# Optimization experiments

Measured on AMD Instinct MI355X. Metric: run time of the kernel, lower is better.

Reference implementation:

```python
import jax, jax.numpy as jnp
import numpy as np

NH, NB, E, R, K, SU = 64, 384, 1024, 1024, 16, 64  # humans, boxes, enc size, repr size, cardinality, sub-repr
C, P, SPA = 256, 7, 36
NUM_ITER = 2


def _ln(x, g, b):
    m = jnp.mean(x, -1, keepdims=True)
    v = jnp.mean((x - m) ** 2, -1, keepdims=True)
    return (x - m) / jnp.sqrt(v + 1e-5) * g + b


def setup_inputs():
    key = jax.random.key(0)
    it = iter(jax.random.split(key, 48))
    def w(shape, scale=0.02):
        return jax.random.normal(next(it), shape, dtype=jnp.float32) * scale
    z = lambda *s: jnp.zeros(s, jnp.float32)
    return {
        "box_feats": jax.random.normal(next(it), (NB, C, P, P), dtype=jnp.float32),
        "spatial_raw": jax.random.uniform(next(it), (NH * NB, SPA), dtype=jnp.float32),
        "features3": jax.random.normal(next(it), (1, C, P, P), dtype=jnp.float32),
        "Wb1": w((C * P * P, E)), "bb1": z(E), "Wb2": w((E, E)), "bb2": z(E),
        "Ws1": w((SPA, 128)), "bs1": z(128), "Ws2": w((128, 256)), "bs2": z(256),
        "Ws3": w((256, 1024)), "bs3": z(1024),
        "Wadj": w((R, 1)), "badj": z(1),
        "gh": jnp.ones((E,), jnp.float32), "bh": z(E),
        "go": jnp.ones((E,), jnp.float32), "bo": z(E),
        "A1": w((K, 2 * E, SU)), "Ab1": z(K, SU), "A2": w((K, 1024, SU)), "Ab2": z(K, SU),
        "A3": w((K, SU, R)), "Ab3": z(K, R),
        "G1": w((K, 256, SU)), "Gb1": z(K, SU), "G2": w((K, 1024, SU)), "Gb2": z(K, SU),
        "G3": w((K, SU, R)), "Gb3": z(K, R),
        "S1": w((K, E, SU)), "Sb1": z(K, SU), "S2": w((K, 1024, SU)), "Sb2": z(K, SU),
        "S3": w((K, SU, R)), "Sb3": z(K, R),
        "O1": w((K, E, SU)), "Ob1": z(K, SU), "O2": w((K, 1024, SU)), "Ob2": z(K, SU),
        "O3": w((K, SU, R)), "Ob3": z(K, R),
        "n_h": NH,
    }


def _forward(box_feats, spatial_raw, features3, Wb1, bb1, Wb2, bb2, Ws1, bs1, Ws2, bs2, Ws3, bs3,
             Wadj, badj, gh, bh, go, bo, A1, Ab1, A2, Ab2, A3, Ab3, G1, Gb1, G2, Gb2, G3, Gb3,
             S1, Sb1, S2, Sb2, S3, Sb3, O1, Ob1, O2, Ob2, O3, Ob3, n_h):
    n = box_feats.shape[0]
    # box_head: Flatten -> Linear -> ReLU -> Linear -> ReLU
    enc = jax.nn.relu(jax.nn.relu(box_feats.reshape(n, -1) @ Wb1 + bb1) @ Wb2 + bb2)  # [n, E]
    h, o = enc[:n_h], enc
    # spatial_head MLP on flat pairs (pair p = i*n + j, human i, object j)
    sp = spatial_raw
    for W, b in ((Ws1, bs1), (Ws2, bs2), (Ws3, bs3)):
        sp = jax.nn.relu(sp @ W + b)                      # [n_h*n, 1024]
    spr = sp.reshape(n_h, n, -1)
    gfeat = features3.mean((2, 3))                        # AdaptiveAvgPool2d(1) -> [1, 256]

    def mbf(app, W1, b1, W2, b2, W3, b3):
        # MultiBranchFusion over flat pairs, K branches vectorized as batched GEMMs
        a = jnp.einsum('pa,kau->kpu', app, W1) + b1[:, None, :]
        s = jnp.einsum('ps,ksu->kpu', sp, W2) + b2[:, None, :]
        m = jax.nn.relu(a * s)                            # [K, P, sub]
        return jax.nn.relu(jnp.einsum('kpu,kur->pr', m, W3) + b3.sum(0))

    def pair_app(hh, oo):
        return jnp.concatenate([jnp.repeat(hh, n, axis=0), jnp.tile(oo, (n_h, 1))], axis=1)

    adj = jnp.ones((n_h, n), sp.dtype)
    for _ in range(NUM_ITER):
        wts = mbf(pair_app(h, o), A1, Ab1, A2, Ab2, A3, Ab3)      # [P, R]
        adj = (wts @ Wadj + badj).reshape(n_h, n)
        # MessageMBF object->subject (_forward_object_nodes): output [n_h, n, R], no final relu
        ao = jnp.einsum('na,kau->knu', o, O1) + Ob1[:, None, :]
        so = jnp.einsum('hns,ksu->khnu', spr, O2) + Ob2[:, None, None, :]
        m_o2s = jnp.einsum('khnu,kur->hnr', jax.nn.relu(ao[:, None] * so), O3) + Ob3.sum(0)
        h = _ln(h + jax.nn.relu(jnp.sum(jax.nn.softmax(adj, 1)[..., None] * m_o2s, axis=1)), gh, bh)
        # MessageMBF subject->object (_forward_human_nodes): output [n, n_h, R]
        ah = jnp.einsum('ha,kau->khu', h, S1) + Sb1[:, None, :]
        sh = jnp.einsum('hns,ksu->khnu', spr, S2) + Sb2[:, None, None, :]
        m_s2o = jnp.einsum('khnu,kur->nhr', jax.nn.relu(ah[:, :, None, :] * sh), S3) + Sb3.sum(0)
        o = _ln(o + jax.nn.relu(jnp.sum(jax.nn.softmax(adj.T, 1)[..., None] * m_s2o, axis=1)), go, bo)

    attn = mbf(pair_app(h, o), A1, Ab1, A2, Ab2, A3, Ab3)          # [P, R]
    gp = jnp.broadcast_to(gfeat, (sp.shape[0], gfeat.shape[1]))
    attn_g = mbf(gp, G1, Gb1, G2, Gb2, G3, Gb3)                    # [P, R]
    return jnp.concatenate([attn, attn_g], axis=1)                 # [P, 2R]


def reference(box_feats, spatial_raw, features3, Wb1, bb1, Wb2, bb2, Ws1, bs1, Ws2, bs2, Ws3, bs3,
              Wadj, badj, gh, bh, go, bo, A1, Ab1, A2, Ab2, A3, Ab3, G1, Gb1, G2, Gb2, G3, Gb3,
              S1, Sb1, S2, Sb2, S3, Sb3, O1, Ob1, O2, Ob2, O3, Ob3, n_h):
    return _forward(box_feats, spatial_raw, features3, Wb1, bb1, Wb2, bb2, Ws1, bs1, Ws2, bs2, Ws3, bs3,
                    Wadj, badj, gh, bh, go, bo, A1, Ab1, A2, Ab2, A3, Ab3, G1, Gb1, G2, Gb2, G3, Gb3,
                    S1, Sb1, S2, Sb2, S3, Sb3, O1, Ob1, O2, Ob2, O3, Ob3, n_h)
```

## Files before the change

### kernel.cpp

```cpp
#include <hip/hip_runtime.h>
#include <hip/hip_bf16.h>
#include <cstdint>
#include <cstddef>

#define NH    64
#define NB    384
#define EDIM  1024
#define PAIRS (NH*NB)
#define SPA   36

using in_t  = float;
using out_t = float;
using sb_t  = __hip_bfloat16;

typedef short bf16x8 __attribute__((ext_vector_type(8)));
typedef float f32x4  __attribute__((ext_vector_type(4)));

static __device__ __forceinline__ float cvt(float x){ return x; }
static __device__ __forceinline__ float cvt(__hip_bfloat16 x){ return __bfloat162float(x); }
static __device__ __forceinline__ void stv(float* p, float v){ *p = v; }
static __device__ __forceinline__ void stv(__hip_bfloat16* p, float v){ *p = __float2bfloat16(v); }

static __device__ __forceinline__ float b2f(unsigned short u){
  union { unsigned int i; float f; } x; x.i = ((unsigned int)u)<<16; return x.f;
}

typedef const __attribute__((address_space(1))) void* as1_t;
typedef __attribute__((address_space(3))) void* as3_t;
static __device__ __forceinline__ void gl_lds16(const void* g, void* l){
  __builtin_amdgcn_global_load_lds((as1_t)g, (as3_t)l, 16, 0, 0);
}

#define POOL_BB1   0
#define POOL_BB2   1024
#define POOL_BS1   2048
#define POOL_BS2   2176
#define POOL_BS3   2432
#define POOL_AB1   3456
#define POOL_GB1   4480
#define POOL_SB1   5504
#define POOL_OB1   6528
#define POOL_B2ALL 7552
#define POOL_AB3S  11648
#define POOL_GB3S  12672
#define POOL_SB3S  13696
#define POOL_OB3S  14720
#define POOL_GFEAT 15744
#define POOL_TOTAL 16000

template<int EPI, int RELU, typename TC>
__global__ __launch_bounds__(256)
void gemm_mfma(int M, int N, int KS, int lda, int ldb,
               const sb_t* __restrict__ A,
               const sb_t* __restrict__ Bt,
               const float* __restrict__ bias,
               TC* __restrict__ C, int ldc, int coff, long long strideCz,
               const float* __restrict__ Wadj,
               const float* __restrict__ ab3s,
               float* __restrict__ adjOut)
{
  __shared__ alignas(16) short lA[2][128*32];
  __shared__ alignas(16) short lB[2][128*32];
  const int tid = threadIdx.x;
  const int w = tid >> 6, l = tid & 63;
  const int m0 = blockIdx.x * 128, n0 = blockIdx.y * 128;
  const int wr = w >> 1, wc = w & 1;
  const int Koff = blockIdx.z * KS;

  const int srow = w*32 + (l>>2);
  const int scol = (l&3)*8;
  const sb_t* gA = A  + (size_t)(m0 + srow)*(size_t)lda + Koff + scol;
  const sb_t* gB = Bt + (size_t)(n0 + srow)*(size_t)ldb + Koff + scol;
  short* lA0 = &lA[0][(w*32)*32];
  short* lA1 = &lA[1][(w*32)*32];
  short* lB0 = &lB[0][(w*32)*32];
  short* lB1 = &lB[1][(w*32)*32];

  f32x4 acc[4][4];
  const f32x4 zz = {0.f,0.f,0.f,0.f};
  #pragma unroll
  for (int i=0;i<4;++i)
    #pragma unroll
    for (int j=0;j<4;++j) acc[i][j] = zz;

  const int fr  = l & 15;
  const int fko = (l >> 4) * 8;

  for (int k0 = 0; k0 < KS; k0 += 64) {
    gl_lds16(gA + k0,               lA0);
    gl_lds16(gA + k0 + 16*lda,      lA0 + 16*32);
    gl_lds16(gA + k0 + 32,          lA1);
    gl_lds16(gA + k0 + 32 + 16*lda, lA1 + 16*32);
    gl_lds16(gB + k0,               lB0);
    gl_lds16(gB + k0 + 16*ldb,      lB0 + 16*32);
    gl_lds16(gB + k0 + 32,          lB1);
    gl_lds16(gB + k0 + 32 + 16*ldb, lB1 + 16*32);
    __syncthreads();
    #pragma unroll
    for (int kh=0; kh<2; ++kh) {
      bf16x8 af[4], bfv[4];
      #pragma unroll
      for (int i=0;i<4;++i)
        af[i]  = *(const bf16x8*)&lA[kh][(wr*64 + i*16 + fr)*32 + fko];
      #pragma unroll
      for (int j=0;j<4;++j)
        bfv[j] = *(const bf16x8*)&lB[kh][(wc*64 + j*16 + fr)*32 + fko];
      #pragma unroll
      for (int i=0;i<4;++i)
        #pragma unroll
        for (int j=0;j<4;++j)
          acc[i][j] = __builtin_amdgcn_mfma_f32_16x16x32_bf16(af[i], bfv[j], acc[i][j], 0, 0, 0);
    }
    __syncthreads();
  }

  const int cn = l & 15;
  const int cr = (l >> 4) * 4;

  if (EPI == 1) {
    float part[4][4];
    #pragma unroll
    for (int i=0;i<4;++i)
      #pragma unroll
      for (int r=0;r<4;++r) part[i][r] = 0.f;
    #pragma unroll
    for (int j=0;j<4;++j) {
      const int col = n0 + wc*64 + j*16 + cn;
      const float wv = Wadj[col];
      const float bv = ab3s[col];
      #pragma unroll
      for (int i=0;i<4;++i)
        #pragma unroll
        for (int r=0;r<4;++r)
          part[i][r] += fmaxf(acc[i][j][r] + bv, 0.f) * wv;
    }
    #pragma unroll
    for (int m=1;m<16;m<<=1)
      #pragma unroll
      for (int i=0;i<4;++i)
        #pragma unroll
        for (int r=0;r<4;++r)
          part[i][r] += __shfl_xor(part[i][r], m, 64);
    if (cn == 0) {
      #pragma unroll
      for (int i=0;i<4;++i)
        #pragma unroll
        for (int r=0;r<4;++r)
          atomicAdd(&adjOut[m0 + wr*64 + i*16 + cr + r], part[i][r]);
    }
    return;
  }

  #pragma unroll
  for (int j=0;j<4;++j) {
    const int col = n0 + wc*64 + j*16 + cn;
    const float bv = (EPI==0 && bias) ? bias[col] : 0.f;
    #pragma unroll
    for (int i=0;i<4;++i) {
      #pragma unroll
      for (int r=0;r<4;++r) {
        const int row = m0 + wr*64 + i*16 + cr + r;
        float v = acc[i][j][r] + bv;
        if (RELU) v = fmaxf(v, 0.f);
        if (EPI == 2)
          stv(&C[(size_t)blockIdx.z*strideCz + (size_t)row*ldc + col], v);
        else
          stv(&C[(size_t)row*ldc + coff + col], v);
      }
    }
  }
}

template<typename TC>
__global__ __launch_bounds__(256)
void gemm_valu(int M, int N, int K,
               const in_t* __restrict__ S, int ldsS,
               const in_t* __restrict__ B, int ldb, long long strideB,
               const float* __restrict__ bias,
               TC* __restrict__ C, int ldc, int reluOut)
{
  __shared__ float As[16][65];
  __shared__ float Bs[16][68];
  const int z  = blockIdx.z;
  const in_t* Bz = B + (long long)z * strideB;
  const int m0 = blockIdx.x * 64;
  const int n0 = blockIdx.y * 64;
  const int tid = threadIdx.x;
  const int tx = tid & 15;
  const int ty = tid >> 4;

  float acc[4][4];
  #pragma unroll
  for (int i=0;i<4;++i)
    #pragma unroll
    for (int j=0;j<4;++j) acc[i][j]=0.f;

  const int kTiles = (K + 15) >> 4;
  for (int kt=0; kt<kTiles; ++kt) {
    const int k0 = kt << 4;
    #pragma unroll
    for (int q=0;q<4;++q) {
      const int p = m0 + ty + 16*q;
      const int c = k0 + tx;
      As[tx][ty+16*q] = (p < M && c < K) ? S[(size_t)p*ldsS + c] : 0.f;
    }
    {
      const int n = tid & 63;
      #pragma unroll
      for (int q=0;q<4;++q) {
        const int kk = (tid >> 6) + 4*q;
        const int gk = k0 + kk;
        const int gn = n0 + n;
        Bs[kk][n] = (gk < K && gn < N) ? Bz[(size_t)gk*ldb + gn] : 0.f;
      }
    }
    __syncthreads();
    #pragma unroll
    for (int kk=0; kk<16; ++kk) {
      float a[4], b[4];
      #pragma unroll
      for (int i=0;i<4;++i) a[i] = As[kk][ty + 16*i];
      #pragma unroll
      for (int j=0;j<4;++j) b[j] = Bs[kk][tx + 16*j];
      #pragma unroll
      for (int i=0;i<4;++i)
        #pragma unroll
        for (int j=0;j<4;++j) acc[i][j] += a[i]*b[j];
    }
    __syncthreads();
  }
  #pragma unroll
  for (int i=0;i<4;++i) {
    const int r = m0 + ty + 16*i;
    if (r >= M) continue;
    #pragma unroll
    for (int j=0;j<4;++j) {
      const int nn = n0 + tx + 16*j;
      if (nn >= N) continue;
      const int ccol = z*N + nn;
      float v = acc[i][j];
      if (bias) v += bias[ccol];
      if (reluOut) v = fmaxf(v, 0.f);
      stv(&C[(size_t)r*ldc + ccol], v);
    }
  }
}

struct Prep17 { const in_t* p[17]; };

__global__ __launch_bounds__(256)
void prep_kernel(Prep17 a, float* __restrict__ pool)
{
  const int len[17] = {1024,1024,128,256,1024,1024,1024,1024,1024,1024,1024,1024,1024,
                       1024,1024,1024,1024};
  const int off[17] = {POOL_BB1,POOL_BB2,POOL_BS1,POOL_BS2,POOL_BS3,POOL_AB1,
                       POOL_B2ALL+0,
                       POOL_GB1,
                       POOL_B2ALL+3072,
                       POOL_SB1,
                       POOL_B2ALL+2048,
                       POOL_OB1,
                       POOL_B2ALL+1024,
                       POOL_AB3S,POOL_GB3S,POOL_SB3S,POOL_OB3S};
  const int j = blockIdx.x;
  const in_t* src = a.p[j];
  const int L = len[j], o = off[j];
  for (int i = threadIdx.x; i < L; i += blockDim.x) {
    if (j < 13) {
      pool[o+i] = src[i];
    } else {
      float s = 0.f;
      for (int k=0;k<16;++k) s += src[k*1024 + i];
      pool[o+i] = s;
    }
  }
}

__global__ __launch_bounds__(64)
void gfeat_kernel(const in_t* __restrict__ f3, float* __restrict__ g)
{
  const int c = blockIdx.x;
  const int t = threadIdx.x;
  float s = (t < 49) ? f3[c*49 + t] : 0.f;
  #pragma unroll
  for (int o=32;o>0;o>>=1) s += __shfl_down(s, o, 64);
  if (t == 0) g[c] = s * (1.0f/49.0f);
}

__global__ __launch_bounds__(256)
void tcvt_kernel(const float* __restrict__ in, sb_t* __restrict__ outT, int R, int C)
{
  __shared__ float t[64][65];
  const int r0 = blockIdx.x*64, c0 = blockIdx.y*64;
  const int x = threadIdx.x & 63, y = threadIdx.x >> 6;
  #pragma unroll 4
  for (int q=0;q<16;++q){ const int rl = q*4 + y; t[rl][x] = in[(size_t)(r0+rl)*C + c0 + x]; }
  __syncthreads();
  #pragma unroll 4
  for (int q=0;q<16;++q){ const int cl = q*4 + y; stv(&outT[(size_t)(c0+cl)*R + r0 + x], t[x][cl]); }
}

__global__ __launch_bounds__(256)
void pack_kt_kernel(const float* __restrict__ W, sb_t* __restrict__ PT, int Cdim)
{
  __shared__ float t[64][65];
  const int c0 = blockIdx.x*64; const int k = blockIdx.y;
  const int x = threadIdx.x & 63, y = threadIdx.x >> 6;
  #pragma unroll 4
  for (int q=0;q<16;++q){ const int cl = q*4 + y; t[cl][x] = W[((size_t)k*Cdim + c0 + cl)*64 + x]; }
  __syncthreads();
  #pragma unroll 4
  for (int q=0;q<16;++q){ const int u = q*4 + y; stv(&PT[((size_t)k*64 + u)*Cdim + c0 + x], t[x][u]); }
}

__global__ void cvt_kernel(const float* __restrict__ in, sb_t* __restrict__ o, int n){
  const int i = blockIdx.x*256 + threadIdx.x;
  if (i < n) stv(&o[i], in[i]);
}

__global__ __launch_bounds__(256)
void combine4_kernel(const float* __restrict__ part, const float* __restrict__ bias,
                     sb_t* __restrict__ o)
{
  const int i = blockIdx.x*256 + threadIdx.x;
  const int c = i & 1023;
  float v = part[i] + part[i+393216] + part[i+2*393216] + part[i+3*393216] + bias[c];
  stv(&o[i], fmaxf(v, 0.f));
}

__global__ __launch_bounds__(256)
void encpost_kernel(const float* __restrict__ oB, sb_t* __restrict__ oBb,
                    float* __restrict__ hB, sb_t* __restrict__ hBb)
{
  const int p = blockIdx.x; const int c = blockIdx.y*256 + threadIdx.x;
  const float v = oB[(size_t)p*1024 + c];
  stv(&oBb[(size_t)p*1024+c], v);
  if (p < NH){ hB[(size_t)p*1024+c] = v; stv(&hBb[(size_t)p*1024+c], v); }
}

__global__ __launch_bounds__(256)
void mmake_kernel(const float* __restrict__ U, int hasU, int ldu,
                  const float* __restrict__ V, int hasV,
                  const sb_t* __restrict__ S, int ldS, int colOff,
                  sb_t* __restrict__ Mo)
{
  const int p = blockIdx.x;
  const int c = threadIdx.x * 4;
  const ushort4 sv = *(const ushort4*)((const unsigned short*)S + (size_t)p*ldS + colOff + c);
  float a0=0.f,a1=0.f,a2=0.f,a3=0.f;
  if (hasU){ const float* Up = U + (size_t)(p/NB)*ldu + c; a0=Up[0];a1=Up[1];a2=Up[2];a3=Up[3]; }
  if (hasV){ const float* Vp = V + (size_t)(p%NB)*1024 + c; a0+=Vp[0];a1+=Vp[1];a2+=Vp[2];a3+=Vp[3]; }
  __hip_bfloat16* mo = (__hip_bfloat16*)Mo + (size_t)p*1024 + c;
  mo[0] = __float2bfloat16(fmaxf(a0*b2f(sv.x),0.f));
  mo[1] = __float2bfloat16(fmaxf(a1*b2f(sv.y),0.f));
  mo[2] = __float2bfloat16(fmaxf(a2*b2f(sv.z),0.f));
  mo[3] = __float2bfloat16(fmaxf(a3*b2f(sv.w),0.f));
}

__global__ __launch_bounds__(512)
void smax_h_kernel(const float* __restrict__ adj, float* __restrict__ wh)
{
  __shared__ float red[512];
  const int hh = blockIdx.x, t = threadIdx.x;
  float av = (t < NB) ? adj[hh*NB + t] : -1e30f;
  red[t]=av; __syncthreads();
  for (int s=256;s>0;s>>=1){ if(t<s) red[t]=fmaxf(red[t],red[t+s]); __syncthreads(); }
  float mx = red[0]; __syncthreads();
  float e = (t < NB) ? __expf(av - mx) : 0.f;
  red[t]=e; __syncthreads();
  for (int s=256;s>0;s>>=1){ if(t<s) red[t]+=red[t+s]; __syncthreads(); }
  if (t < NB) wh[hh*NB + t] = e / red[0];
}

__global__ __launch_bounds__(64)
void smax_o_kernel(const float* __restrict__ adj, float* __restrict__ wo)
{
  const int n = blockIdx.x, t = threadIdx.x;
  float av = adj[t*NB + n];
  float mx = av;
  #pragma unroll
  for (int o=32;o>0;o>>=1) mx = fmaxf(mx, __shfl_xor(mx, o, 64));
  float e = __expf(av - mx);
  float s = e;
  #pragma unroll
  for (int o=32;o>0;o>>=1) s += __shfl_xor(s, o, 64);
  wo[n*64 + t] = e / s;
}

__global__ __launch_bounds__(128)
void wredH_kernel(const float* __restrict__ wh, const float* __restrict__ ao,
                  const sb_t* __restrict__ s4, int colOff, sb_t* __restrict__ mw)
{
  const int hh = blockIdx.x;
  const int c = blockIdx.y*128 + threadIdx.x;
  const unsigned short* sp = (const unsigned short*)s4 + (size_t)hh*NB*4096 + colOff + c;
  const float* whp = wh + hh*NB;
  float acc = 0.f;
  for (int n=0; n<NB; ++n)
    acc += whp[n] * fmaxf(ao[(size_t)n*1024 + c] * b2f(sp[(size_t)n*4096]), 0.f);
  stv(&mw[(size_t)hh*1024 + c], acc);
}

__global__ __launch_bounds__(128)
void wredO_kernel(const float* __restrict__ wo, const float* __restrict__ ah,
                  const sb_t* __restrict__ s4, int colOff, sb_t* __restrict__ mw)
{
  const int n = blockIdx.x;
  const int c = blockIdx.y*128 + threadIdx.x;
  const unsigned short* sp = (const unsigned short*)s4 + (size_t)n*4096 + colOff + c;
  const float* wop = wo + n*64;
  float acc = 0.f;
  for (int h=0; h<NH; ++h)
    acc += wop[h] * fmaxf(ah[(size_t)h*1024 + c] * b2f(sp[(size_t)h*NB*4096]), 0.f);
  stv(&mw[(size_t)n*1024 + c], acc);
}

static __device__ __forceinline__ float bsum(float v, float* red){
  const int t = threadIdx.x;
  red[t]=v; __syncthreads();
  for (int s=512;s>0;s>>=1){ if(t<s) red[t]+=red[t+s]; __syncthreads(); }
  float r = red[0]; __syncthreads();
  return r;
}

__global__ __launch_bounds__(1024)
void ln_update_kernel(const float* __restrict__ msg, const float* __restrict__ b3s,
                      const in_t* __restrict__ g, const in_t* __restrict__ b,
                      float* __restrict__ x, sb_t* __restrict__ xb)
{
  __shared__ float red[1024];
  const int row = blockIdx.x, t = threadIdx.x;
  float val = x[(size_t)row*1024 + t] + fmaxf(msg[(size_t)row*1024 + t] + b3s[t], 0.f);
  float mean = bsum(val, red) * (1.0f/1024.0f);
  float d = val - mean;
  float var = bsum(d*d, red) * (1.0f/1024.0f);
  float y = d * rsqrtf(var + 1e-5f) * g[t] + b[t];
  x[(size_t)row*1024 + t] = y;
  stv(&xb[(size_t)row*1024 + t], y);
}

template<int EPI, int RELU, typename TC>
static inline void launch_mfma(hipStream_t st, int M, int N, int KS, int lda, int ldb, int nz,
    const sb_t* A, const sb_t* Bt, const float* bias, TC* C, int ldc, int coff,
    long long strideCz, const float* Wadj, const float* ab3s, float* adjOut)
{
  dim3 g((unsigned)(M/128), (unsigned)(N/128), (unsigned)nz);
  hipLaunchKernelGGL((gemm_mfma<EPI,RELU,TC>), g, dim3(256), 0, st,
                     M,N,KS,lda,ldb,A,Bt,bias,C,ldc,coff,strideCz,Wadj,ab3s,adjOut);
}

extern "C" void kernel_launch(void* const* d_in, const int* in_sizes, int n_in,
                              void* d_out, int out_size, void* d_ws, size_t ws_size,
                              hipStream_t stream)
{
  (void)in_sizes; (void)n_in; (void)out_size; (void)ws_size;

  const in_t* box  = (const in_t*)d_in[0];
  const in_t* spat = (const in_t*)d_in[1];
  const in_t* f3   = (const in_t*)d_in[2];
  const in_t* Wb1  = (const in_t*)d_in[3];
  const in_t* Wb2  = (const in_t*)d_in[5];
  const in_t* Ws1  = (const in_t*)d_in[7];
  const in_t* Ws2  = (const in_t*)d_in[9];
  const in_t* Ws3  = (const in_t*)d_in[11];
  const in_t* Wadj = (const in_t*)d_in[13];
  const in_t* gh   = (const in_t*)d_in[15];
  const in_t* bh   = (const in_t*)d_in[16];
  const in_t* go   = (const in_t*)d_in[17];
  const in_t* bo   = (const in_t*)d_in[18];
  const in_t* A1   = (const in_t*)d_in[19];
  const in_t* A2   = (const in_t*)d_in[21];
  const in_t* A3   = (const in_t*)d_in[23];
  const in_t* G1   = (const in_t*)d_in[25];
  const in_t* G2   = (const in_t*)d_in[27];
  const in_t* G3   = (const in_t*)d_in[29];
  const in_t* S1   = (const in_t*)d_in[31];
  const in_t* S2   = (const in_t*)d_in[33];
  const in_t* S3   = (const in_t*)d_in[35];
  const in_t* O1   = (const in_t*)d_in[37];
  const in_t* O2   = (const in_t*)d_in[39];
  const in_t* O3   = (const in_t*)d_in[41];
  out_t* out = (out_t*)d_out;

  char* wsb = (char*)d_ws;
  size_t off = 0;
  auto alloc = [&](size_t bytes)->void* {
    void* p = wsb + off; off += (bytes + 255) & ~(size_t)255; return p;
  };
  float* pool   = (float*)alloc((size_t)POOL_TOTAL*4);
  sb_t* Wb1T    = (sb_t*)alloc((size_t)1024*12544*2);
  sb_t* Wb2T    = (sb_t*)alloc((size_t)1024*1024*2);
  sb_t* Ws2T    = (sb_t*)alloc((size_t)256*128*2);
  sb_t* Ws3T    = (sb_t*)alloc((size_t)1024*256*2);
  sb_t* A3T     = (sb_t*)alloc((size_t)1024*1024*2);
  sb_t* O3T     = (sb_t*)alloc((size_t)1024*1024*2);
  sb_t* S3T     = (sb_t*)alloc((size_t)1024*1024*2);
  sb_t* G3T     = (sb_t*)alloc((size_t)1024*1024*2);
  sb_t* s2Tall  = (sb_t*)alloc((size_t)4096*1024*2);
  sb_t* O1T     = (sb_t*)alloc((size_t)1024*1024*2);
  sb_t* S1T     = (sb_t*)alloc((size_t)1024*1024*2);
  sb_t* A1T     = (sb_t*)alloc((size_t)1024*2048*2);
  sb_t* boxb    = (sb_t*)alloc((size_t)NB*12544*2);
  float* encP   = (float*)alloc((size_t)4*NB*EDIM*4);
  sb_t* encMidb = (sb_t*)alloc((size_t)NB*EDIM*2);
  float* oB     = (float*)alloc((size_t)NB*EDIM*4);
  sb_t* oBb     = (sb_t*)alloc((size_t)NB*EDIM*2);
  float* hB     = (float*)alloc((size_t)NH*EDIM*4);
  sb_t* hBb     = (sb_t*)alloc((size_t)128*EDIM*2);
  sb_t* sp1b    = (sb_t*)alloc((size_t)PAIRS*128*2);
  sb_t* sp2b    = (sb_t*)alloc((size_t)PAIRS*256*2);
  sb_t* spFb    = (sb_t*)alloc((size_t)PAIRS*EDIM*2);
  sb_t* mbuf    = spFb;
  sb_t* s4      = (sb_t*)alloc((size_t)PAIRS*4096*2);
  float* ahA    = (float*)alloc((size_t)128*EDIM*4);
  float* aoA    = (float*)alloc((size_t)NB*EDIM*4);
  float* aoO    = (float*)alloc((size_t)NB*EDIM*4);
  float* ahS    = (float*)alloc((size_t)128*EDIM*4);
  float* aGv    = (float*)alloc((size_t)EDIM*4);
  float* adj    = (float*)alloc((size_t)PAIRS*4);
  float* wh     = (float*)alloc((size_t)PAIRS*4);
  float* wo     = (float*)alloc((size_t)PAIRS*4);
  sb_t* mwH     = (sb_t*)alloc((size_t)128*EDIM*2);
  sb_t* mwO     = (sb_t*)alloc((size_t)NB*EDIM*2);
  float* hmsg   = (float*)alloc((size_t)128*EDIM*4);
  float* omsg   = (float*)alloc((size_t)NB*EDIM*4);

  Prep17 pp;
  const int prepIdx[17] = {4,6,8,10,12,20,22,26,28,32,34,38,40,24,30,36,42};
  for (int i=0;i<17;++i) pp.p[i] = (const in_t*)d_in[prepIdx[i]];
  hipLaunchKernelGGL(prep_kernel, dim3(17), dim3(256), 0, stream, pp, pool);
  hipLaunchKernelGGL(gfeat_kernel, dim3(256), dim3(64), 0, stream, f3, pool + POOL_GFEAT);

  hipLaunchKernelGGL(tcvt_kernel, dim3(196,16), dim3(256), 0, stream, Wb1, Wb1T, 12544, 1024);
  hipLaunchKernelGGL(tcvt_kernel, dim3(16,16),  dim3(256), 0, stream, Wb2, Wb2T, 1024, 1024);
  hipLaunchKernelGGL(tcvt_kernel, dim3(2,4),    dim3(256), 0, stream, Ws2, Ws2T, 128, 256);
  hipLaunchKernelGGL(tcvt_kernel, dim3(4,16),   dim3(256), 0, stream, Ws3, Ws3T, 256, 1024);
  hipLaunchKernelGGL(tcvt_kernel, dim3(16,16),  dim3(256), 0, stream, A3, A3T, 1024, 1024);
  hipLaunchKernelGGL(tcvt_kernel, dim3(16,16),  dim3(256), 0, stream, O3, O3T, 1024, 1024);
  hipLaunchKernelGGL(tcvt_kernel, dim3(16,16),  dim3(256), 0, stream, S3, S3T, 1024, 1024);
  hipLaunchKernelGGL(tcvt_kernel, dim3(16,16),  dim3(256), 0, stream, G3, G3T, 1024, 1024);

  hipLaunchKernelGGL(pack_kt_kernel, dim3(16,16), dim3(256), 0, stream, A2, s2Tall,            1024);
  hipLaunchKernelGGL(pack_kt_kernel, dim3(16,16), dim3(256), 0, stream, O2, s2Tall+1024*1024,  1024);
  hipLaunchKernelGGL(pack_kt_kernel, dim3(16,16), dim3(256), 0, stream, S2, s2Tall+2048*1024,  1024);
  hipLaunchKernelGGL(pack_kt_kernel, dim3(16,16), dim3(256), 0, stream, G2, s2Tall+3072*1024,  1024);
  hipLaunchKernelGGL(pack_kt_kernel, dim3(16,16), dim3(256), 0, stream, O1, O1T, 1024);
  hipLaunchKernelGGL(pack_kt_kernel, dim3(16,16), dim3(256), 0, stream, S1, S1T, 1024);
  hipLaunchKernelGGL(pack_kt_kernel, dim3(32,16), dim3(256), 0, stream, A1, A1T, 2048);

  hipLaunchKernelGGL(cvt_kernel, dim3((NB*12544)/256), dim3(256), 0, stream, box, boxb, NB*12544);

  launch_mfma<2,0,float>(stream, NB, EDIM, 3136, 12544, 12544, 4,
      boxb, Wb1T, nullptr, encP, EDIM, 0, (long long)NB*EDIM, nullptr, nullptr, nullptr);
  hipLaunchKernelGGL(combine4_kernel, dim3(NB*EDIM/256), dim3(256), 0, stream,
                     encP, pool+POOL_BB1, encMidb);
  launch_mfma<0,1,float>(stream, NB, EDIM, EDIM, EDIM, EDIM, 1,
      encMidb, Wb2T, pool+POOL_BB2, oB, EDIM, 0, 0, nullptr, nullptr, nullptr);
  hipLaunchKernelGGL(encpost_kernel, dim3(NB,4), dim3(256), 0, stream, oB, oBb, hB, hBb);

  {
    dim3 g((PAIRS+63)/64, 2, 1);
    hipLaunchKernelGGL((gemm_valu<sb_t>), g, dim3(256), 0, stream,
        PAIRS, 128, SPA, spat, SPA, Ws1, 128, 0, pool+POOL_BS1, sp1b, 128, 1);
  }
  launch_mfma<0,1,sb_t>(stream, PAIRS, 256, 128, 128, 128, 1,
      sp1b, Ws2T, pool+POOL_BS2, sp2b, 256, 0, 0, nullptr, nullptr, nullptr);
  launch_mfma<0,1,sb_t>(stream, PAIRS, EDIM, 256, 256, 256, 1,
      sp2b, Ws3T, pool+POOL_BS3, spFb, EDIM, 0, 0, nullptr, nullptr, nullptr);

  launch_mfma<0,0,sb_t>(stream, PAIRS, 4096, EDIM, EDIM, EDIM, 1,
      spFb, s2Tall, pool+POOL_B2ALL, s4, 4096, 0, 0, nullptr, nullptr, nullptr);

  {
    dim3 g(1, 1, 16);
    hipLaunchKernelGGL((gemm_valu<float>), g, dim3(256), 0, stream,
        1, 64, 256, pool+POOL_GFEAT, 256, G1, 64, 16384, pool+POOL_GB1, aGv, EDIM, 0);
  }

  for (int it=0; it<2; ++it) {
    launch_mfma<0,0,float>(stream, 128, EDIM, EDIM, EDIM, 2048, 1,
        hBb, A1T, pool+POOL_AB1, ahA, EDIM, 0, 0, nullptr, nullptr, nullptr);
    launch_mfma<0,0,float>(stream, NB, EDIM, EDIM, EDIM, 2048, 1,
        oBb, A1T+1024, nullptr, aoA, EDIM, 0, 0, nullptr, nullptr, nullptr);
    hipLaunchKernelGGL(mmake_kernel, dim3(PAIRS), dim3(256), 0, stream,
                       ahA, 1, 1024, aoA, 1, s4, 4096, 0, mbuf);
    hipMemsetAsync(adj, 0, (size_t)PAIRS*4, stream);
    launch_mfma<1,0,float>(stream, PAIRS, EDIM, EDIM, EDIM, EDIM, 1,
        mbuf, A3T, nullptr, (float*)nullptr, 0, 0, 0, Wadj, pool+POOL_AB3S, adj);
    hipLaunchKernelGGL(smax_h_kernel, dim3(NH), dim3(512), 0, stream, adj, wh);
    hipLaunchKernelGGL(smax_o_kernel, dim3(NB), dim3(64), 0, stream, adj, wo);

    launch_mfma<0,0,float>(stream, NB, EDIM, EDIM, EDIM, EDIM, 1,
        oBb, O1T, pool+POOL_OB1, aoO, EDIM, 0, 0, nullptr, nullptr, nullptr);
    hipLaunchKernelGGL(wredH_kernel, dim3(NH,8), dim3(128), 0, stream,
                       wh, aoO, s4, 1024, mwH);
    launch_mfma<0,0,float>(stream, 128, EDIM, EDIM, EDIM, EDIM, 1,
        mwH, O3T, nullptr, hmsg, EDIM, 0, 0, nullptr, nullptr, nullptr);
    hipLaunchKernelGGL(ln_update_kernel, dim3(NH), dim3(1024), 0, stream,
                       hmsg, pool+POOL_OB3S, gh, bh, hB, hBb);

    launch_mfma<0,0,float>(stream, 128, EDIM, EDIM, EDIM, EDIM, 1,
        hBb, S1T, pool+POOL_SB1, ahS, EDIM, 0, 0, nullptr, nullptr, nullptr);
    hipLaunchKernelGGL(wredO_kernel, dim3(NB,8), dim3(128), 0, stream,
                       wo, ahS, s4, 2048, mwO);
    launch_mfma<0,0,float>(stream, NB, EDIM, EDIM, EDIM, EDIM, 1,
        mwO, S3T, nullptr, omsg, EDIM, 0, 0, nullptr, nullptr, nullptr);
    hipLaunchKernelGGL(ln_update_kernel, dim3(NB), dim3(1024), 0, stream,
                       omsg, pool+POOL_SB3S, go, bo, oB, oBb);
  }

  launch_mfma<0,0,float>(stream, 128, EDIM, EDIM, EDIM, 2048, 1,
      hBb, A1T, pool+POOL_AB1, ahA, EDIM, 0, 0, nullptr, nullptr, nullptr);
  launch_mfma<0,0,float>(stream, NB, EDIM, EDIM, EDIM, 2048, 1,
      oBb, A1T+1024, nullptr, aoA, EDIM, 0, 0, nullptr, nullptr, nullptr);
  hipLaunchKernelGGL(mmake_kernel, dim3(PAIRS), dim3(256), 0, stream,
                     ahA, 1, 1024, aoA, 1, s4, 4096, 0, mbuf);
  launch_mfma<0,1,out_t>(stream, PAIRS, EDIM, EDIM, EDIM, EDIM, 1,
      mbuf, A3T, pool+POOL_AB3S, out, 2048, 0, 0, nullptr, nullptr, nullptr);

  hipLaunchKernelGGL(mmake_kernel, dim3(PAIRS), dim3(256), 0, stream,
                     aGv, 1, 0, nullptr, 0, s4, 4096, 3072, mbuf);
  launch_mfma<0,1,out_t>(stream, PAIRS, EDIM, EDIM, EDIM, EDIM, 1,
      mbuf, G3T, pool+POOL_GB3S, out, 2048, 1024, 0, nullptr, nullptr, nullptr);
}
```

Before: 1.709 ms.

## Add 256x256-tile MFMA GEMM with phased LDS pipelining for large pair GEMMs

Adds a new 512-thread GEMM kernel with 256x256 output tiles. It double-buffers LDS with direct global-to-LDS loads staged in quarter-tile phases, uses XCD-aware workgroup remapping, and raises MFMA priority during compute. The large pair-sized GEMMs (spatial head, s4 projection, adjacency and final output GEMMs) are switched to it, aiming to increase operand reuse and hide load latency. The cost is higher register and LDS pressure, a grid with fewer blocks, and reliance on dimensions divisible by 256.

Measured after the change: 1.682 ms. Within noise of the previous version (-1.6%).

```diff
diff --git a/kernel.cpp b/kernel.cpp
--- a/kernel.cpp
+++ b/kernel.cpp
@@ -166,6 +166,197 @@
           stv(&C[(size_t)blockIdx.z*strideCz + (size_t)row*ldc + col], v);
         else
           stv(&C[(size_t)row*ldc + coff + col], v);
+      }
+    }
+  }
+}
+
+template<int EPI, int RELU, typename TC>
+__global__ __launch_bounds__(512, 2)
+void gemm256(int M, int N, int K, int lda, int ldb,
+             const sb_t* __restrict__ A,
+             const sb_t* __restrict__ Bt,
+             const float* __restrict__ bias,
+             TC* __restrict__ C, int ldc, int coff,
+             const float* __restrict__ Wadj,
+             const float* __restrict__ ab3s,
+             float* __restrict__ adjOut)
+{
+  __shared__ alignas(16) short sh[2][2][256*64];
+
+  const int tid = threadIdx.x;
+  const int w = tid >> 6, l = tid & 63;
+  const int wr = w >> 2, wc = w & 3;
+
+  const unsigned gx = gridDim.x, gy = gridDim.y;
+  const unsigned nwg = gx * gy;
+  const unsigned hwid = blockIdx.x + gx * blockIdx.y;
+  const unsigned q = nwg >> 3, rr = nwg & 7;
+  const unsigned xcd = hwid & 7, jj = hwid >> 3;
+  const unsigned wg = (xcd < rr ? xcd*(q+1) : rr*(q+1) + (xcd-rr)*q) + jj;
+  const int by = (int)(wg % gy), bx = (int)(wg / gy);
+  const int m0 = bx * 256, n0 = by * 256;
+
+  const int NT = K >> 6;
+
+  const int lr = l >> 3;
+  const int lch = ((l & 7) ^ lr) * 8;
+
+  auto stage = [&](int p, int s, int t){
+    short* lbA = &sh[p][0][0];
+    short* lbB = &sh[p][1][0];
+    const int k0 = t * 64;
+    #pragma unroll
+    for (int c=0;c<2;++c){
+      const int g = (w<<1) + c;
+      int row0; const sb_t* mat; int ld; int rb; short* dst;
+      if (s==0){ row0 = g*8;                              mat=Bt; ld=ldb; rb=n0; dst=lbB; }
+      else if (s==1){ row0 = 128 + g*8;                   mat=Bt; ld=ldb; rb=n0; dst=lbB; }
+      else if (s==2){ row0 = (g<8)? g*8    : 128+(g-8)*8; mat=A;  ld=lda; rb=m0; dst=lbA; }
+      else          { row0 = (g<8)? 64+g*8 : 192+(g-8)*8; mat=A;  ld=lda; rb=m0; dst=lbA; }
+      gl_lds16(mat + (size_t)(rb + row0 + lr)*(size_t)ld + k0 + lch, dst + row0*64);
+    }
+  };
+
+  const int fr = l & 15;
+  const int fg = l >> 4;
+  const int sx = fr & 7;
+  const int x0 = ((0 + fg) ^ sx) * 8;
+  const int x1 = ((4 + fg) ^ sx) * 8;
+  const int oA = (wr*128 + fr) * 64;
+  const int oB = (wc*64  + fr) * 64;
+
+  f32x4 acc[8][4];
+  const f32x4 zz = {0.f,0.f,0.f,0.f};
+  #pragma unroll
+  for (int i=0;i<8;++i)
+    #pragma unroll
+    for (int j=0;j<4;++j) acc[i][j] = zz;
+
+#define G256_BAR()   __builtin_amdgcn_s_barrier()
+#define G256_LGKM0() asm volatile("s_waitcnt lgkmcnt(0)" ::: "memory")
+#define G256_LGKM8() asm volatile("s_waitcnt lgkmcnt(8)" ::: "memory")
+#define G256_VM(n)   asm volatile("s_waitcnt vmcnt(" #n ")" ::: "memory")
+#define G256_LOADA(ph)                                                   \
+  af[0][0] = *(const bf16x8*)(sa + oA + (2*(ph)+0)*1024 + x0);           \
+  af[0][1] = *(const bf16x8*)(sa + oA + (2*(ph)+0)*1024 + x1);           \
+  af[1][0] = *(const bf16x8*)(sa + oA + (2*(ph)+1)*1024 + x0);           \
+  af[1][1] = *(const bf16x8*)(sa + oA + (2*(ph)+1)*1024 + x1)
+#define G256_MFMA(ph)                                                    \
+  do { __builtin_amdgcn_s_setprio(1);                                    \
+    _Pragma("unroll") for (int ii=0; ii<2; ++ii)                         \
+    _Pragma("unroll") for (int j=0; j<4; ++j)                            \
+    _Pragma("unroll") for (int kk=0; kk<2; ++kk)                         \
+      acc[2*(ph)+ii][j] = __builtin_amdgcn_mfma_f32_16x16x32_bf16(       \
+          af[ii][kk], bf[j][kk], acc[2*(ph)+ii][j], 0, 0, 0);            \
+    __builtin_amdgcn_s_setprio(0); } while(0)
+
+  stage(0,0,0); stage(0,1,0); stage(0,2,0); stage(0,3,0);
+  G256_VM(4);
+  if (NT > 1) {
+    stage(1,0,1); stage(1,1,1); stage(1,2,1);
+    G256_VM(6);
+  } else {
+    G256_VM(0);
+  }
+  G256_BAR();
+
+  for (int t=0; t<NT; ++t) {
+    const int cur = t & 1, pn = cur ^ 1;
+    short* sa  = &sh[cur][0][0];
+    short* sb2 = &sh[cur][1][0];
+    bf16x8 bf[4][2], af[2][2];
+
+    #pragma unroll
+    for (int j=0;j<4;++j){
+      bf[j][0] = *(const bf16x8*)(sb2 + oB + j*1024 + x0);
+      bf[j][1] = *(const bf16x8*)(sb2 + oB + j*1024 + x1);
+    }
+    G256_LOADA(0);
+    if (t+1 < NT) stage(pn, 3, t+1);
+    G256_LGKM8();
+    G256_BAR(); G256_LGKM0();
+    G256_MFMA(0);
+    G256_BAR();
+
+    G256_LOADA(1);
+    if (t+2 < NT) stage(cur, 0, t+2);
+    G256_BAR(); G256_LGKM0();
+    G256_MFMA(1);
+    G256_BAR();
+
+    G256_LOADA(2);
+    if (t+2 < NT) stage(cur, 1, t+2);
+    G256_BAR(); G256_LGKM0();
+    G256_MFMA(2);
+    G256_BAR();
+
+    G256_LOADA(3);
+    if (t+2 < NT) stage(cur, 2, t+2);
+    G256_BAR(); G256_LGKM0();
+    G256_MFMA(3);
+    if (t+1 < NT) {
+      if (t+2 < NT) { G256_VM(6); } else { G256_VM(0); }
+      G256_BAR();
+    }
+  }
+
+#undef G256_BAR
+#undef G256_LGKM0
+#undef G256_LGKM8
+#undef G256_VM
+#undef G256_LOADA
+#undef G256_MFMA
+
+  const int cn = l & 15;
+  const int cr = (l >> 4) * 4;
+
+  if (EPI == 1) {
+    float part[8][4];
+    #pragma unroll
+    for (int i=0;i<8;++i)
+      #pragma unroll
+      for (int r=0;r<4;++r) part[i][r] = 0.f;
+    #pragma unroll
+    for (int j=0;j<4;++j) {
+      const int col = n0 + wc*64 + j*16 + cn;
+      const float wv = Wadj[col];
+      const float bv = ab3s[col];
+      #pragma unroll
+      for (int i=0;i<8;++i)
+        #pragma unroll
+        for (int r=0;r<4;++r)
+          part[i][r] += fmaxf(acc[i][j][r] + bv, 0.f) * wv;
+    }
+    #pragma unroll
+    for (int m=1;m<16;m<<=1)
+      #pragma unroll
+      for (int i=0;i<8;++i)
+        #pragma unroll
+        for (int r=0;r<4;++r)
+          part[i][r] += __shfl_xor(part[i][r], m, 64);
+    if (cn == 0) {
+      #pragma unroll
+      for (int i=0;i<8;++i)
+        #pragma unroll
+        for (int r=0;r<4;++r)
+          atomicAdd(&adjOut[m0 + wr*128 + i*16 + cr + r], part[i][r]);
+    }
+    return;
+  }
+
+  #pragma unroll
+  for (int j=0;j<4;++j) {
+    const int col = n0 + wc*64 + j*16 + cn;
+    const float bv = bias ? bias[col] : 0.f;
+    #pragma unroll
+    for (int i=0;i<8;++i) {
+      #pragma unroll
+      for (int r=0;r<4;++r) {
+        const int row = m0 + wr*128 + i*16 + cr + r;
+        float v = acc[i][j][r] + bv;
+        if (RELU) v = fmaxf(v, 0.f);
+        stv(&C[(size_t)row*ldc + coff + col], v);
       }
     }
   }
@@ -447,6 +638,16 @@
   dim3 g((unsigned)(M/128), (unsigned)(N/128), (unsigned)nz);
   hipLaunchKernelGGL((gemm_mfma<EPI,RELU,TC>), g, dim3(256), 0, st,
                      M,N,KS,lda,ldb,A,Bt,bias,C,ldc,coff,strideCz,Wadj,ab3s,adjOut);
+}
+
+template<int EPI, int RELU, typename TC>
+static inline void launch_mfma256(hipStream_t st, int M, int N, int K, int lda, int ldb,
+    const sb_t* A, const sb_t* Bt, const float* bias, TC* C, int ldc, int coff,
+    const float* Wadj, const float* ab3s, float* adjOut)
+{
+  dim3 g((unsigned)(M/256), (unsigned)(N/256), 1);
+  hipLaunchKernelGGL((gemm256<EPI,RELU,TC>), g, dim3(512), 0, st,
+                     M,N,K,lda,ldb,A,Bt,bias,C,ldc,coff,Wadj,ab3s,adjOut);
 }
 
 extern "C" void kernel_launch(void* const* d_in, const int* in_sizes, int n_in,
@@ -565,11 +766,11 @@
   }
   launch_mfma<0,1,sb_t>(stream, PAIRS, 256, 128, 128, 128, 1,
       sp1b, Ws2T, pool+POOL_BS2, sp2b, 256, 0, 0, nullptr, nullptr, nullptr);
-  launch_mfma<0,1,sb_t>(stream, PAIRS, EDIM, 256, 256, 256, 1,
-      sp2b, Ws3T, pool+POOL_BS3, spFb, EDIM, 0, 0, nullptr, nullptr, nullptr);
-
-  launch_mfma<0,0,sb_t>(stream, PAIRS, 4096, EDIM, EDIM, EDIM, 1,
-      spFb, s2Tall, pool+POOL_B2ALL, s4, 4096, 0, 0, nullptr, nullptr, nullptr);
+  launch_mfma256<0,1,sb_t>(stream, PAIRS, EDIM, 256, 256, 256,
+      sp2b, Ws3T, pool+POOL_BS3, spFb, EDIM, 0, nullptr, nullptr, nullptr);
+
+  launch_mfma256<0,0,sb_t>(stream, PAIRS, 4096, EDIM, EDIM, EDIM,
+      spFb, s2Tall, pool+POOL_B2ALL, s4, 4096, 0, nullptr, nullptr, nullptr);
 
   {
     dim3 g(1, 1, 16);
@@ -584,9 +785,9 @@
         oBb, A1T+1024, nullptr, aoA, EDIM, 0, 0, nullptr, nullptr, nullptr);
     hipLaunchKernelGGL(mmake_kernel, dim3(PAIRS), dim3(256), 0, stream,
                        ahA, 1, 1024, aoA, 1, s4, 4096, 0, mbuf);
-    hipMemsetAsync(adj, 0, (size_t)PAIRS*4, stream);
-    launch_mfma<1,0,float>(stream, PAIRS, EDIM, EDIM, EDIM, EDIM, 1,
-        mbuf, A3T, nullptr, (float*)nullptr, 0, 0, 0, Wadj, pool+POOL_AB3S, adj);
+    (void)hipMemsetAsync(adj, 0, (size_t)PAIRS*4, stream);
+    launch_mfma256<1,0,float>(stream, PAIRS, EDIM, EDIM, EDIM, EDIM,
+        mbuf, A3T, nullptr, (float*)nullptr, 0, 0, Wadj, pool+POOL_AB3S, adj);
     hipLaunchKernelGGL(smax_h_kernel, dim3(NH), dim3(512), 0, stream, adj, wh);
     hipLaunchKernelGGL(smax_o_kernel, dim3(NB), dim3(64), 0, stream, adj, wo);
 
@@ -615,11 +816,11 @@
       oBb, A1T+1024, nullptr, aoA, EDIM, 0, 0, nullptr, nullptr, nullptr);
   hipLaunchKernelGGL(mmake_kernel, dim3(PAIRS), dim3(256), 0, stream,
                      ahA, 1, 1024, aoA, 1, s4, 4096, 0, mbuf);
-  launch_mfma<0,1,out_t>(stream, PAIRS, EDIM, EDIM, EDIM, EDIM, 1,
-      mbuf, A3T, pool+POOL_AB3S, out, 2048, 0, 0, nullptr, nullptr, nullptr);
+  launch_mfma256<0,1,out_t>(stream, PAIRS, EDIM, EDIM, EDIM, EDIM,
+      mbuf, A3T, pool+POOL_AB3S, out, 2048, 0, nullptr, nullptr, nullptr);
 
   hipLaunchKernelGGL(mmake_kernel, dim3(PAIRS), dim3(256), 0, stream,
                      aGv, 1, 0, nullptr, 0, s4, 4096, 3072, mbuf);
-  launch_mfma<0,1,out_t>(stream, PAIRS, EDIM, EDIM, EDIM, EDIM, 1,
-      mbuf, G3T, pool+POOL_GB3S, out, 2048, 1024, 0, nullptr, nullptr, nullptr);
-}
+  launch_mfma256<0,1,out_t>(stream, PAIRS, EDIM, EDIM, EDIM, EDIM,
+      mbuf, G3T, pool+POOL_GB3S, out, 2048, 1024, nullptr, nullptr, nullptr);
+}
```
